# Optimization experiments

Measured on AMD Instinct MI355X. Metric: run time of the kernel, lower is better.

The kernel has to match this reference:

```python
import jax, jax.numpy as jnp
import numpy as np

B, T, C, H = 4, 2048, 1024, 16
D = C // H  # head_dim = 64

def setup_inputs() -> dict:
    key = jax.random.key(0)
    ks = jax.random.split(key, 5)
    s = 0.02
    return {
        "x": jax.random.normal(ks[0], (B, T, C), dtype=jnp.float32),
        "W_attn": jax.random.normal(ks[1], (C, 3 * C), dtype=jnp.float32) * s,
        "b_attn": jnp.zeros((3 * C,), dtype=jnp.float32),
        "W_proj": jax.random.normal(ks[2], (C, C), dtype=jnp.float32) * s,
        "b_proj": jnp.zeros((C,), dtype=jnp.float32),
    }

def reference(x, W_attn, b_attn, W_proj, b_proj):
    Bx, Tx, Cx = x.shape
    qkv = x @ W_attn + b_attn                       # [B,T,3C]
    q, k, v = jnp.split(qkv, 3, axis=-1)
    def heads(t):
        return t.reshape(Bx, Tx, H, D).transpose(0, 2, 1, 3)  # [B,H,T,D]
    Q, K, V = heads(q), heads(k), heads(v)
    scale = 1.0 / np.sqrt(D).astype(np.float32)
    att = jnp.einsum('bhqd,bhkd->bhqk', Q, K) * scale        # [B,H,T,T]
    causal = jnp.tril(jnp.ones((Tx, Tx), dtype=bool))
    att = jnp.where(causal[None, None], att, -jnp.inf)
    att = jax.nn.softmax(att, axis=-1)
    y = jnp.einsum('bhqk,bhkd->bhqd', att, V)                # [B,H,T,D]
    y = y.transpose(0, 2, 1, 3).reshape(Bx, Tx, Cx)
    return y @ W_proj + b_proj
```

## Files before the change

kernel.cpp:

```cpp
#include <hip/hip_runtime.h>
#include <hip/hip_bf16.h>

#define B_ 4
#define T_ 2048
#define C_ 1024
#define H_ 16
#define D_ 64

using u16x4 = __attribute__((ext_vector_type(4))) unsigned short;
using u16x8 = __attribute__((ext_vector_type(8))) unsigned short;
using s16x8 = __attribute__((ext_vector_type(8))) short;
using f32x4v = __attribute__((ext_vector_type(4))) float;
using f32x16 = __attribute__((ext_vector_type(16))) float;

__device__ inline float bf2f(unsigned short u) {
  return __uint_as_float(((unsigned int)u) << 16);
}
__device__ inline unsigned short f2bf(float f) {
  unsigned int x = __float_as_uint(f);
  unsigned int r = (x + 0x7fffu + ((x >> 16) & 1u)) >> 16;
  return (unsigned short)r;
}
__device__ inline float fexp2(float x) {
  float r;
  asm("v_exp_f32 %0, %1" : "=v"(r) : "v"(x));
  return r;
}

__device__ inline unsigned cvtpk_bf16(float lo, float hi) {
  unsigned r;
  asm("v_cvt_pk_bf16_f32 %0, %1, %2" : "=v"(r) : "v"(lo), "v"(hi));
  return r;
}

__device__ inline s16x8 repack8(float p0, float p1, float p2, float p3,
                                float p4, float p5, float p6, float p7) {
  unsigned w0 = cvtpk_bf16(p0, p1), w1 = cvtpk_bf16(p2, p3);
  unsigned w2 = cvtpk_bf16(p4, p5), w3 = cvtpk_bf16(p6, p7);
  asm volatile("v_permlane32_swap_b32 %0, %1" : "+v"(w0), "+v"(w2));
  asm volatile("v_permlane32_swap_b32 %0, %1" : "+v"(w1), "+v"(w3));
  union { unsigned u[4]; s16x8 v; } r;
  r.u[0] = w0; r.u[1] = w1; r.u[2] = w2; r.u[3] = w3;
  return r.v;
}

__global__ __launch_bounds__(256) void cast_f32_bf16(const float* __restrict__ in,
                                                     ushort* __restrict__ out, int n4) {
  const int stride = gridDim.x * blockDim.x;
  for (int i = blockIdx.x * blockDim.x + threadIdx.x; i < n4; i += stride) {
    float4 v = ((const float4*)in)[i];
    u16x4 o = {f2bf(v.x), f2bf(v.y), f2bf(v.z), f2bf(v.w)};
    ((u16x4*)out)[i] = o;
  }
}

__global__ __launch_bounds__(256) void transpose_cast(const float* __restrict__ W,
                                                      ushort* __restrict__ Wt, int K, int N) {
  __shared__ float tile[64][65];
  const int n0 = blockIdx.x * 64, k0 = blockIdx.y * 64;
  const int tid = threadIdx.x;
  const int tr = tid >> 4, tc4 = (tid & 15) * 4;
#pragma unroll
  for (int i = 0; i < 4; ++i) {
    int r = tr + i * 16;
    float4 v = *(const float4*)&W[(size_t)(k0 + r) * N + n0 + tc4];
    tile[r][tc4 + 0] = v.x; tile[r][tc4 + 1] = v.y;
    tile[r][tc4 + 2] = v.z; tile[r][tc4 + 3] = v.w;
  }
  __syncthreads();
#pragma unroll
  for (int i = 0; i < 4; ++i) {
    int n = tr + i * 16;
    u16x4 o;
#pragma unroll
    for (int j = 0; j < 4; ++j) o[j] = f2bf(tile[tc4 + j][n]);
    *(u16x4*)&Wt[(size_t)(n0 + n) * K + k0 + tc4] = o;
  }
}

template <int BF16OUT, int NT>
__global__ __launch_bounds__(256) void gemm_bt(const ushort* __restrict__ A,
                                               const ushort* __restrict__ Bt,
                                               const float* __restrict__ bias,
                                               void* __restrict__ Cout,
                                               int M, int N, int K) {
  constexpr int BM = 128, BN = 128, BK = 64;
  __shared__ ushort Alds[BM * BK];
  __shared__ ushort Blds[BN * BK];
  const int tid = threadIdx.x;
  const int lane = tid & 63;
  const int w = tid >> 6;
  const int wr = w >> 1, wc = w & 1;
  const int nlin = blockIdx.y * gridDim.x + blockIdx.x;
  const int cpx = (gridDim.x * gridDim.y) >> 3;
  const int swzb = (nlin & 7) * cpx + (nlin >> 3);
  const int m0 = (swzb / gridDim.x) * BM;
  const int njbase = swzb % gridDim.x;

  const int ra = w * 32 + (lane >> 3);
  const int ca = (lane & 7) * 8;

  for (int tt = 0; tt < NT; ++tt) {
    const int n0 = (njbase + tt * gridDim.x) * BN;
    f32x4v acc[4][4] = {};

    for (int k0 = 0; k0 < K; k0 += BK) {
#pragma unroll
      for (int i = 0; i < 4; ++i) {
        const ushort* ga = A + (size_t)(m0 + ra + i * 8) * K + k0 + ca;
        __builtin_amdgcn_global_load_lds(
            (const __attribute__((address_space(1))) void*)ga,
            (__attribute__((address_space(3))) void*)&Alds[w * 2048 + i * 512], 16, 0, 0);
        const ushort* gb = Bt + (size_t)(n0 + ra + i * 8) * K + k0 + ca;
        __builtin_amdgcn_global_load_lds(
            (const __attribute__((address_space(1))) void*)gb,
            (__attribute__((address_space(3))) void*)&Blds[w * 2048 + i * 512], 16, 0, 0);
      }
      __syncthreads();
#pragma unroll
      for (int ks = 0; ks < 2; ++ks) {
        s16x8 af[4], bfr[4];
#pragma unroll
        for (int m = 0; m < 4; ++m)
          af[m] = *(const s16x8*)&Alds[(wr * 64 + m * 16 + (lane & 15)) * BK + ks * 32 + ((lane >> 4) * 8)];
#pragma unroll
        for (int n = 0; n < 4; ++n)
          bfr[n] = *(const s16x8*)&Blds[(wc * 64 + n * 16 + (lane & 15)) * BK + ks * 32 + ((lane >> 4) * 8)];
#pragma unroll
        for (int m = 0; m < 4; ++m)
#pragma unroll
          for (int n = 0; n < 4; ++n)
            acc[m][n] = __builtin_amdgcn_mfma_f32_16x16x32_bf16(af[m], bfr[n], acc[m][n], 0, 0, 0);
      }
      __syncthreads();
    }

#pragma unroll
    for (int m = 0; m < 4; ++m) {
      const int rg = m0 + wr * 64 + m * 16 + ((lane >> 4) * 4);
#pragma unroll
      for (int n = 0; n < 4; ++n) {
        const int cg = n0 + wc * 64 + n * 16 + (lane & 15);
        const float bv = bias[cg];
#pragma unroll
        for (int r2 = 0; r2 < 4; ++r2) {
          float v = acc[m][n][r2] + bv;
          if constexpr (BF16OUT)
            ((ushort*)Cout)[(size_t)(rg + r2) * N + cg] = f2bf(v);
          else
            ((float*)Cout)[(size_t)(rg + r2) * N + cg] = v;
        }
      }
    }
  }
}

__global__ __launch_bounds__(256, 4) void attn_kernel(const ushort* __restrict__ qkv,
                                                      ushort* __restrict__ y) {
  constexpr int C3 = 3 * C_;
  const int n = blockIdx.x;
  const int c = n & 7;
  const int j = n >> 3;
  const int hbl = j & 7;
  const int qt = ((j >> 3) + hbl) & 15;
  const int hb = c * 8 + hbl;
  const int h = hb >> 2, b = hb & 3;
  const int tid = threadIdx.x;
  const int lane = tid & 63;
  const int w = tid >> 6;
  const int hi = lane >> 5;
  const int l31 = lane & 31;

  __shared__ __align__(16) ushort Klds[3][64 * 64];
  __shared__ __align__(16) ushort Vt[2][64 * 64];

  const int s_slot0 = (w * 2 + 0) * 1024 + lane * 16;
  const int s_slot1 = (w * 2 + 1) * 1024 + lane * 16;
  const int s_row0 = s_slot0 >> 7, s_row1 = s_slot1 >> 7;
  const int s_col0 = ((s_slot0 & 127) ^ ((s_row0 & 7) << 4)) >> 1;
  const int s_col1 = ((s_slot1 & 127) ^ ((s_row1 & 7) << 4)) >> 1;
  const ushort* kbase = qkv + (size_t)(b * T_) * C3 + C_ + h * D_;
  const ushort* vbase = qkv + (size_t)(b * T_) * C3 + 2 * C_ + h * D_;

  const int kv0 = l31 * 2;
  const int vdb = ((w << 1) | hi) * 8;

  s16x8 qf[4];
  {
    const ushort* qr = qkv + (size_t)(b * T_ + qt * 128 + w * 32 + l31) * C3 + h * D_;
#pragma unroll
    for (int ds = 0; ds < 4; ++ds) {
      s16x8 v = *(const s16x8*)(qr + ds * 16 + hi * 8);
#pragma unroll
      for (int jj = 0; jj < 8; ++jj)
        v[jj] = (short)f2bf(bf2f((unsigned short)v[jj]) * 0.18033688f);
      qf[ds] = v;
    }
  }

  const int ntile = 2 * qt + 2;
  const int nt_w = 2 * qt + 1 + (w >> 1);

  __builtin_amdgcn_global_load_lds(
      (const __attribute__((address_space(1))) void*)(kbase + (size_t)s_row0 * C3 + s_col0),
      (__attribute__((address_space(3))) void*)&Klds[0][(w * 2 + 0) * 512], 16, 0, 0);
  __builtin_amdgcn_global_load_lds(
      (const __attribute__((address_space(1))) void*)(kbase + (size_t)s_row1 * C3 + s_col1),
      (__attribute__((address_space(3))) void*)&Klds[0][(w * 2 + 1) * 512], 16, 0, 0);
  u16x8 vnA = *(const u16x8*)(vbase + (size_t)kv0 * C3 + vdb);
  u16x8 vnB = *(const u16x8*)(vbase + (size_t)(kv0 + 1) * C3 + vdb);
  if (ntile > 1) {
    __builtin_amdgcn_global_load_lds(
        (const __attribute__((address_space(1))) void*)(kbase + (size_t)(64 + s_row0) * C3 + s_col0),
        (__attribute__((address_space(3))) void*)&Klds[1][(w * 2 + 0) * 512], 16, 0, 0);
    __builtin_amdgcn_global_load_lds(
        (const __attribute__((address_space(1))) void*)(kbase + (size_t)(64 + s_row1) * C3 + s_col1),
        (__attribute__((address_space(3))) void*)&Klds[1][(w * 2 + 1) * 512], 16, 0, 0);
  }
#pragma unroll
  for (int jj = 0; jj < 8; ++jj) {
    int d = vdb + jj;
    *(unsigned*)&Vt[0][d * 64 + (kv0 ^ ((d & 7) << 3))] =
        (unsigned)vnA[jj] | ((unsigned)vnB[jj] << 16);
  }
  asm volatile("s_waitcnt lgkmcnt(0)" ::: "memory");
  __builtin_amdgcn_s_barrier();
  asm volatile("" ::: "memory");

  f32x16 yacc0 = {}, yacc1 = {};
  float lrun = 0.f;
  const int qg = qt * 128 + w * 32 + l31;

  int kcur = 0, vcur = 0;
  for (int t = 0; t < ntile; ++t) {
    const bool m1 = (t + 1 < ntile);
    const bool m2 = (t + 2 < ntile);
    if (m1) {
      const ushort* vrow = vbase + (size_t)((t + 1) * 64 + kv0) * C3;
      vnA = *(const u16x8*)(vrow + vdb);
      vnB = *(const u16x8*)(vrow + C3 + vdb);
    }
    if (m2) {
      const int kb2 = kcur >= 1 ? kcur - 1 : 2;
      __builtin_amdgcn_global_load_lds(
          (const __attribute__((address_space(1))) void*)(kbase + (size_t)((t + 2) * 64 + s_row0) * C3 + s_col0),
          (__attribute__((address_space(3))) void*)&Klds[kb2][(w * 2 + 0) * 512], 16, 0, 0);
      __builtin_amdgcn_global_load_lds(
          (const __attribute__((address_space(1))) void*)(kbase + (size_t)((t + 2) * 64 + s_row1) * C3 + s_col1),
          (__attribute__((address_space(3))) void*)&Klds[kb2][(w * 2 + 1) * 512], 16, 0, 0);
    }

    if (t < nt_w) {
      const bool diag = (t == nt_w - 1);
      const bool has_kb1 = (!diag) || ((w & 1) == 1);

      f32x16 sv0 = {}, sv1 = {};
      __builtin_amdgcn_s_setprio(1);
      {
        const int swr = (l31 & 7) << 3;
#pragma unroll
        for (int ds = 0; ds < 4; ++ds) {
          s16x8 kf = *(const s16x8*)&Klds[kcur][l31 * 64 + ((ds * 16 + hi * 8) ^ swr)];
          sv0 = __builtin_amdgcn_mfma_f32_32x32x16_bf16(kf, qf[ds], sv0, 0, 0, 0);
        }
      }
      if (has_kb1) {
        const int row = l31 + 32;
        const int swr = (row & 7) << 3;
#pragma unroll
        for (int ds = 0; ds < 4; ++ds) {
          s16x8 kf = *(const s16x8*)&Klds[kcur][row * 64 + ((ds * 16 + hi * 8) ^ swr)];
          sv1 = __builtin_amdgcn_mfma_f32_32x32x16_bf16(kf, qf[ds], sv1, 0, 0, 0);
        }
      }
      __builtin_amdgcn_s_setprio(0);

      if (diag) {
        const int kb0 = t * 64 + (w & 1) * 32 + 4 * hi;
        if ((w & 1) == 0) {
#pragma unroll
          for (int r = 0; r < 16; ++r)
            if (kb0 + (r & 3) + 8 * (r >> 2) > qg) sv0[r] = -1e30f;
        } else {
#pragma unroll
          for (int r = 0; r < 16; ++r)
            if (kb0 + (r & 3) + 8 * (r >> 2) > qg) sv1[r] = -1e30f;
        }
      }

      float l0_ = 0.f, l1_ = 0.f, l2_ = 0.f, l3_ = 0.f;
#pragma unroll
      for (int r = 0; r < 16; r += 4) {
        float p0v = fexp2(sv0[r]), p1v = fexp2(sv0[r + 1]);
        float p2v = fexp2(sv0[r + 2]), p3v = fexp2(sv0[r + 3]);
        sv0[r] = p0v; sv0[r + 1] = p1v; sv0[r + 2] = p2v; sv0[r + 3] = p3v;
        l0_ += p0v; l1_ += p1v; l2_ += p2v; l3_ += p3v;
      }
      if (has_kb1) {
#pragma unroll
        for (int r = 0; r < 16; r += 4) {
          float p0v = fexp2(sv1[r]), p1v = fexp2(sv1[r + 1]);
          float p2v = fexp2(sv1[r + 2]), p3v = fexp2(sv1[r + 3]);
          sv1[r] = p0v; sv1[r + 1] = p1v; sv1[r + 2] = p2v; sv1[r + 3] = p3v;
          l0_ += p0v; l1_ += p1v; l2_ += p2v; l3_ += p3v;
        }
      }
      float ls = (l0_ + l1_) + (l2_ + l3_);
      ls += __shfl_xor(ls, 32);
      lrun += ls;

      s16x8 pa0 = repack8(sv0[0], sv0[1], sv0[2], sv0[3], sv0[4], sv0[5], sv0[6], sv0[7]);
      s16x8 pa1 = repack8(sv0[8], sv0[9], sv0[10], sv0[11], sv0[12], sv0[13], sv0[14], sv0[15]);
      s16x8 pa2 = {}, pa3 = {};
      if (has_kb1) {
        pa2 = repack8(sv1[0], sv1[1], sv1[2], sv1[3], sv1[4], sv1[5], sv1[6], sv1[7]);
        pa3 = repack8(sv1[8], sv1[9], sv1[10], sv1[11], sv1[12], sv1[13], sv1[14], sv1[15]);
      }

      __builtin_amdgcn_s_setprio(1);
#pragma unroll
      for (int db = 0; db < 2; ++db) {
        const int d = db * 32 + l31;
        const int swz = (d & 7) << 3;
        s16x8 vf0 = *(const s16x8*)&Vt[vcur][d * 64 + ((0 + hi * 8) ^ swz)];
        s16x8 vf1 = *(const s16x8*)&Vt[vcur][d * 64 + ((16 + hi * 8) ^ swz)];
        if (db == 0) {
          yacc0 = __builtin_amdgcn_mfma_f32_32x32x16_bf16(vf0, pa0, yacc0, 0, 0, 0);
          yacc0 = __builtin_amdgcn_mfma_f32_32x32x16_bf16(vf1, pa1, yacc0, 0, 0, 0);
        } else {
          yacc1 = __builtin_amdgcn_mfma_f32_32x32x16_bf16(vf0, pa0, yacc1, 0, 0, 0);
          yacc1 = __builtin_amdgcn_mfma_f32_32x32x16_bf16(vf1, pa1, yacc1, 0, 0, 0);
        }
        if (has_kb1) {
          s16x8 vf2 = *(const s16x8*)&Vt[vcur][d * 64 + ((32 + hi * 8) ^ swz)];
          s16x8 vf3 = *(const s16x8*)&Vt[vcur][d * 64 + ((48 + hi * 8) ^ swz)];
          if (db == 0) {
            yacc0 = __builtin_amdgcn_mfma_f32_32x32x16_bf16(vf2, pa2, yacc0, 0, 0, 0);
            yacc0 = __builtin_amdgcn_mfma_f32_32x32x16_bf16(vf3, pa3, yacc0, 0, 0, 0);
          } else {
            yacc1 = __builtin_amdgcn_mfma_f32_32x32x16_bf16(vf2, pa2, yacc1, 0, 0, 0);
            yacc1 = __builtin_amdgcn_mfma_f32_32x32x16_bf16(vf3, pa3, yacc1, 0, 0, 0);
          }
        }
      }
      __builtin_amdgcn_s_setprio(0);
    }

    if (m1) {
#pragma unroll
      for (int jj = 0; jj < 8; ++jj) {
        int d = vdb + jj;
        *(unsigned*)&Vt[vcur ^ 1][d * 64 + (kv0 ^ ((d & 7) << 3))] =
            (unsigned)vnA[jj] | ((unsigned)vnB[jj] << 16);
      }
    }
    asm volatile("s_waitcnt lgkmcnt(0)" ::: "memory");
    __builtin_amdgcn_s_barrier();
    asm volatile("" ::: "memory");
    kcur = kcur == 2 ? 0 : kcur + 1;
    vcur ^= 1;
  }

  {
    const float inv = 1.f / lrun;
    yacc0 = yacc0 * inv;
    yacc1 = yacc1 * inv;
    ushort* tile = ((ushort*)Klds) + w * 2048;
    const int swq = (l31 & 7) << 3;
#pragma unroll
    for (int q4 = 0; q4 < 4; ++q4) {
      u16x4 p0, p1;
#pragma unroll
      for (int i = 0; i < 4; ++i) {
        p0[i] = f2bf(yacc0[q4 * 4 + i]);
        p1[i] = f2bf(yacc1[q4 * 4 + i]);
      }
      const int db0 = 8 * q4 + 4 * hi;
      *(u16x4*)&tile[l31 * 64 + (db0 ^ swq)] = p0;
      *(u16x4*)&tile[l31 * 64 + ((db0 + 32) ^ swq)] = p1;
    }
    const int eq = lane >> 1;
    const int ecb = (lane & 1) * 32;
    const int esz = (eq & 7) << 3;
    ushort* dst = y + (size_t)(b * T_ + qt * 128 + w * 32 + eq) * C_ + h * D_ + ecb;
#pragma unroll
    for (int cc = 0; cc < 4; ++cc) {
      u16x8 v = *(const u16x8*)&tile[eq * 64 + ((ecb + cc * 8) ^ esz)];
      *(u16x8*)(dst + cc * 8) = v;
    }
  }
}

extern "C" void kernel_launch(void* const* d_in, const int* in_sizes, int n_in,
                              void* d_out, int out_size, void* d_ws, size_t ws_size,
                              hipStream_t stream) {
  const float* x = (const float*)d_in[0];
  const float* W_attn = (const float*)d_in[1];
  const float* b_attn = (const float*)d_in[2];
  const float* W_proj = (const float*)d_in[3];
  const float* b_proj = (const float*)d_in[4];
  float* out = (float*)d_out;

  char* ws = (char*)d_ws;
  ushort* xb   = (ushort*)(ws);
  ushort* Wta  = (ushort*)(ws + (size_t)16777216);
  ushort* Wtp  = (ushort*)(ws + (size_t)23068672);
  ushort* qkvb = (ushort*)(ws + (size_t)25165824);
  ushort* yb   = (ushort*)(ws + (size_t)75497472);

  cast_f32_bf16<<<2048, 256, 0, stream>>>(x, xb, (B_ * T_ * C_) / 4);
  transpose_cast<<<dim3(48, 16), 256, 0, stream>>>(W_attn, Wta, C_, 3 * C_);
  transpose_cast<<<dim3(16, 16), 256, 0, stream>>>(W_proj, Wtp, C_, C_);
  gemm_bt<1, 3><<<dim3(8, 64), 256, 0, stream>>>(xb, Wta, b_attn, (void*)qkvb,
                                                 B_ * T_, 3 * C_, C_);
  attn_kernel<<<dim3(1024), 256, 0, stream>>>(qkvb, yb);
  gemm_bt<0, 1><<<dim3(8, 64), 256, 0, stream>>>(yb, Wtp, b_proj, (void*)out,
                                                 B_ * T_, C_, C_);
}
```

Before: 197.2 us.

## Double-buffer GEMM LDS tiles and XOR-swizzle LDS layout

```diff
diff --git a/kernel.cpp b/kernel.cpp
--- a/kernel.cpp
+++ b/kernel.cpp
@@ -85,8 +85,8 @@
                                                void* __restrict__ Cout,
                                                int M, int N, int K) {
   constexpr int BM = 128, BN = 128, BK = 64;
-  __shared__ ushort Alds[BM * BK];
-  __shared__ ushort Blds[BN * BK];
+  __shared__ ushort Alds[2][BM * BK];
+  __shared__ ushort Blds[2][BN * BK];
   const int tid = threadIdx.x;
   const int lane = tid & 63;
   const int w = tid >> 6;
@@ -98,41 +98,60 @@
   const int njbase = swzb % gridDim.x;
 
   const int ra = w * 32 + (lane >> 3);
-  const int ca = (lane & 7) * 8;
+  const int ca = ((lane & 7) * 8) ^ ((lane >> 3) << 3);
+  const int swzr = (lane & 15 & 7) << 3;
+  const int ko8 = (lane >> 4) * 8;
+  const int l15 = lane & 15;
+
+#define GB_STAGE(KK, BUF)                                                              \
+  {                                                                                    \
+    _Pragma("unroll") for (int i = 0; i < 4; ++i) {                                    \
+      const ushort* ga = A + (size_t)(m0 + ra + i * 8) * K + (KK) + ca;                \
+      __builtin_amdgcn_global_load_lds(                                                \
+          (const __attribute__((address_space(1))) void*)ga,                           \
+          (__attribute__((address_space(3))) void*)&Alds[BUF][w * 2048 + i * 512], 16, \
+          0, 0);                                                                       \
+      const ushort* gb = Bt + (size_t)(n0 + ra + i * 8) * K + (KK) + ca;               \
+      __builtin_amdgcn_global_load_lds(                                                \
+          (const __attribute__((address_space(1))) void*)gb,                           \
+          (__attribute__((address_space(3))) void*)&Blds[BUF][w * 2048 + i * 512], 16, \
+          0, 0);                                                                       \
+    }                                                                                  \
+  }
 
   for (int tt = 0; tt < NT; ++tt) {
     const int n0 = (njbase + tt * gridDim.x) * BN;
     f32x4v acc[4][4] = {};
 
+    GB_STAGE(0, 0);
+    asm volatile("s_waitcnt vmcnt(0)" ::: "memory");
+    __builtin_amdgcn_s_barrier();
+    asm volatile("" ::: "memory");
+
+    int cur = 0;
     for (int k0 = 0; k0 < K; k0 += BK) {
-#pragma unroll
-      for (int i = 0; i < 4; ++i) {
-        const ushort* ga = A + (size_t)(m0 + ra + i * 8) * K + k0 + ca;
-        __builtin_amdgcn_global_load_lds(
-            (const __attribute__((address_space(1))) void*)ga,
-            (__attribute__((address_space(3))) void*)&Alds[w * 2048 + i * 512], 16, 0, 0);
-        const ushort* gb = Bt + (size_t)(n0 + ra + i * 8) * K + k0 + ca;
-        __builtin_amdgcn_global_load_lds(
-            (const __attribute__((address_space(1))) void*)gb,
-            (__attribute__((address_space(3))) void*)&Blds[w * 2048 + i * 512], 16, 0, 0);
-      }
-      __syncthreads();
+      if (k0 + BK < K) GB_STAGE(k0 + BK, cur ^ 1);
 #pragma unroll
       for (int ks = 0; ks < 2; ++ks) {
         s16x8 af[4], bfr[4];
 #pragma unroll
         for (int m = 0; m < 4; ++m)
-          af[m] = *(const s16x8*)&Alds[(wr * 64 + m * 16 + (lane & 15)) * BK + ks * 32 + ((lane >> 4) * 8)];
+          af[m] = *(const s16x8*)&Alds[cur][(wr * 64 + m * 16 + l15) * BK +
+                                            ((ks * 32 + ko8) ^ swzr)];
 #pragma unroll
         for (int n = 0; n < 4; ++n)
-          bfr[n] = *(const s16x8*)&Blds[(wc * 64 + n * 16 + (lane & 15)) * BK + ks * 32 + ((lane >> 4) * 8)];
+          bfr[n] = *(const s16x8*)&Blds[cur][(wc * 64 + n * 16 + l15) * BK +
+                                             ((ks * 32 + ko8) ^ swzr)];
 #pragma unroll
         for (int m = 0; m < 4; ++m)
 #pragma unroll
           for (int n = 0; n < 4; ++n)
             acc[m][n] = __builtin_amdgcn_mfma_f32_16x16x32_bf16(af[m], bfr[n], acc[m][n], 0, 0, 0);
       }
-      __syncthreads();
+      asm volatile("s_waitcnt vmcnt(0) lgkmcnt(0)" ::: "memory");
+      __builtin_amdgcn_s_barrier();
+      asm volatile("" ::: "memory");
+      cur ^= 1;
     }
 
 #pragma unroll
@@ -140,7 +159,7 @@
       const int rg = m0 + wr * 64 + m * 16 + ((lane >> 4) * 4);
 #pragma unroll
       for (int n = 0; n < 4; ++n) {
-        const int cg = n0 + wc * 64 + n * 16 + (lane & 15);
+        const int cg = n0 + wc * 64 + n * 16 + l15;
         const float bv = bias[cg];
 #pragma unroll
         for (int r2 = 0; r2 < 4; ++r2) {
@@ -153,6 +172,7 @@
       }
     }
   }
+#undef GB_STAGE
 }
 
 __global__ __launch_bounds__(256, 4) void attn_kernel(const ushort* __restrict__ qkv,
```

After: 173.2 us. -12.2%, faster.
